# Kernel optimization log

Hardware: AMD Instinct MI355X
Metric: run time of the kernel (lower is better)

Reference implementation:

```python
import jax, jax.numpy as jnp
import numpy as np

RADIUS = 8
EPS = 0.0001


def box_filter_1d(x, axis, r):
    # cumsum summed-area trick; zero padding at edges (matches torch version)
    cs = jnp.swapaxes(jnp.cumsum(x, axis=axis), axis, 0)
    out = jnp.concatenate([
        cs[r:2 * r + 1],
        cs[2 * r + 1:] - cs[:-2 * r - 1],
        cs[-1:] - cs[-2 * r - 1:-r - 1],
    ], axis=0)
    return jnp.swapaxes(out, 0, axis)


def box_filter(x, r):
    for ax in range(2, x.ndim):
        x = box_filter_1d(x, ax, r)
    return x


def setup_inputs() -> dict:
    key = jax.random.key(0)
    k1, k2 = jax.random.split(key)
    I = jax.random.normal(k1, (8, 4, 768, 768), dtype=jnp.float32)
    p = jax.random.uniform(k2, (8, 1, 768, 768), dtype=jnp.float32)
    return {"I": I, "p": p}


def reference(I, p):
    r = RADIUS
    bs, c, h, w = I.shape
    f = lambda t: box_filter(t, r)

    N = f(jnp.ones_like(I[:, :1]))              # (b,1,h,w) window pixel counts
    I_mean = f(I) / N                            # (b,c,h,w)
    p_mean = f(p) / N                            # (b,1,h,w)
    Ip_mean = f(p * I) / N                       # (b,c,h,w)
    first_term = Ip_mean - p_mean * I_mean       # (b,c,h,w)

    # per-pixel cxc covariance of the guide
    cov = jnp.einsum('bchw,bdhw->bcdhw', I, I).reshape(bs, c * c, h, w)
    cov = (f(cov) / N).reshape(bs, c, c, h, w).transpose(0, 3, 4, 1, 2)  # (b,h,w,c,c)
    eps_mat = EPS * jnp.eye(c, dtype=I.dtype)
    second_term = jnp.linalg.inv(cov + eps_mat)  # batched small-matrix inverse

    # NOTE: einsum strings reproduce the original module exactly
    A = jnp.einsum('bchw,bhwcd->bchw', first_term, second_term)
    b = p_mean - jnp.einsum('bchw,bdhw->bhw', A, I_mean)[:, None]  # (b,1,h,w)

    A_mean = f(A) / N
    b_mean = f(b) / N
    q = jnp.einsum('bchw,bdhw->bhw', A_mean, I)[:, None] + b_mean
    return q
```

## Files before the change

### kernel.cpp

```cpp
#include <hip/hip_runtime.h>


#define HH 768
#define WW 768
#define CC 4
#define BB 8
#define RR 8
#define EPSF 1.0e-4f

#define TA 128
#define OUTA 112
#define SHA 24
#define NSTRIPE (HH / SHA)
#define NBAND 7

#define SHB 16
#define NSTRIPEB (HH / SHB)

__device__ __forceinline__ void loadpix(const float* __restrict__ Ib,
                                        const float* __restrict__ pb,
                                        int row, int gc, float pr[19]) {
  const int off = row * WW + gc;
  const int chs = HH * WW;
  float i0 = Ib[off];
  float i1 = Ib[chs + off];
  float i2 = Ib[2 * chs + off];
  float i3 = Ib[3 * chs + off];
  float pv = pb[off];
  pr[0] = i0; pr[1] = i1; pr[2] = i2; pr[3] = i3;
  pr[4] = pv;
  pr[5] = pv * i0; pr[6] = pv * i1; pr[7] = pv * i2; pr[8] = pv * i3;
  pr[9]  = i0 * i0; pr[10] = i0 * i1; pr[11] = i0 * i2; pr[12] = i0 * i3;
  pr[13] = i1 * i1; pr[14] = i1 * i2; pr[15] = i1 * i3;
  pr[16] = i2 * i2; pr[17] = i2 * i3;
  pr[18] = i3 * i3;
}

__global__ __launch_bounds__(TA) void gf_stageA(const float* __restrict__ I,
                                                const float* __restrict__ p,
                                                float2* __restrict__ AB,
                                                float* __restrict__ sumI_ws,
                                                int storeSum) {
  __shared__ float v[TA][20];
  __shared__ float s4[TA][20];
  const int tid = threadIdx.x;
  const int band0 = (int)blockIdx.x * OUTA;
  const int r0 = (int)blockIdx.y * SHA;
  const int batch = (int)blockIdx.z;
  const int gc = band0 - RR + tid;
  const bool colok = (gc >= 0 && gc < WW);

  const float* Ib = I + (size_t)batch * CC * HH * WW;
  const float* pb = p + (size_t)batch * HH * WW;
  float* sIb = sumI_ws + (size_t)batch * HH * WW;

  float s[20];
#pragma unroll
  for (int k = 0; k < 20; ++k) s[k] = 0.0f;

  if (colok) {
    int rlo = r0 - RR - 1; if (rlo < 0) rlo = 0;
    for (int row = rlo; row < r0 + RR; ++row) {
      float pr[19]; loadpix(Ib, pb, row, gc, pr);
#pragma unroll
      for (int k = 0; k < 19; ++k) s[k] += pr[k];
      if (storeSum && r0 == 0)
        sIb[row * WW + gc] = pr[0] + pr[1] + pr[2] + pr[3];
    }
  }

  const int oc = band0 + tid;
  const bool outok = (tid < OUTA) && (oc < WW);
  const int nw = min(oc + RR, WW - 1) - max(oc - RR, 0) + 1;

  for (int r = r0; r < r0 + SHA; ++r) {
    if (colok) {
      int rl = r + RR;
      if (rl < HH) {
        float pr[19]; loadpix(Ib, pb, rl, gc, pr);
#pragma unroll
        for (int k = 0; k < 19; ++k) s[k] += pr[k];
        if (storeSum)
          sIb[rl * WW + gc] = pr[0] + pr[1] + pr[2] + pr[3];
      }
      int rt = r - RR - 1;
      if (rt >= 0) {
        float pr[19]; loadpix(Ib, pb, rt, gc, pr);
#pragma unroll
        for (int k = 0; k < 19; ++k) s[k] -= pr[k];
      }
    }
    {
      float4* vp = (float4*)(&v[tid][0]);
      vp[0] = make_float4(s[0],  s[1],  s[2],  s[3]);
      vp[1] = make_float4(s[4],  s[5],  s[6],  s[7]);
      vp[2] = make_float4(s[8],  s[9],  s[10], s[11]);
      vp[3] = make_float4(s[12], s[13], s[14], s[15]);
      vp[4] = make_float4(s[16], s[17], s[18], 0.0f);
    }
    __syncthreads();
    float t4[20];
    if (tid < TA - 3) {
      const float* a1 = &v[tid + 1][0];
      const float* a2 = &v[tid + 2][0];
      const float* a3 = &v[tid + 3][0];
      float4* op = (float4*)(&s4[tid][0]);
#pragma unroll
      for (int j = 0; j < 5; ++j) {
        float4 xa = ((const float4*)a1)[j];
        float4 xb = ((const float4*)a2)[j];
        float4 xc = ((const float4*)a3)[j];
        float o0 = s[4*j + 0] + xa.x + xb.x + xc.x;
        float o1 = s[4*j + 1] + xa.y + xb.y + xc.y;
        float o2 = s[4*j + 2] + xa.z + xb.z + xc.z;
        float o3 = s[4*j + 3] + xa.w + xb.w + xc.w;
        op[j] = make_float4(o0, o1, o2, o3);
        t4[4*j + 0] = o0; t4[4*j + 1] = o1; t4[4*j + 2] = o2; t4[4*j + 3] = o3;
      }
    }
    __syncthreads();
    if (outok) {
      float h[20];
      const float* q4  = &s4[tid + 4][0];
      const float* q8  = &s4[tid + 8][0];
      const float* q12 = &s4[tid + 12][0];
      const float* q16 = &v[tid + 16][0];
#pragma unroll
      for (int j = 0; j < 5; ++j) {
        float4 a4 = ((const float4*)q4)[j];
        float4 b4 = ((const float4*)q8)[j];
        float4 c4 = ((const float4*)q12)[j];
        float4 d4 = ((const float4*)q16)[j];
        h[4*j + 0] = t4[4*j + 0] + a4.x + b4.x + c4.x + d4.x;
        h[4*j + 1] = t4[4*j + 1] + a4.y + b4.y + c4.y + d4.y;
        h[4*j + 2] = t4[4*j + 2] + a4.z + b4.z + c4.z + d4.z;
        h[4*j + 3] = t4[4*j + 3] + a4.w + b4.w + c4.w + d4.w;
      }
      const int nh = min(r + RR, HH - 1) - max(r - RR, 0) + 1;
      const float invN = 1.0f / (float)(nh * nw);
      float Im0 = h[0] * invN, Im1 = h[1] * invN, Im2 = h[2] * invN, Im3 = h[3] * invN;
      float pm = h[4] * invN;
      float ft0 = h[5] * invN - pm * Im0;
      float ft1 = h[6] * invN - pm * Im1;
      float ft2 = h[7] * invN - pm * Im2;
      float ft3 = h[8] * invN - pm * Im3;
      float m[4][4];
      m[0][0] = h[9]  * invN + EPSF;
      m[0][1] = h[10] * invN;
      m[0][2] = h[11] * invN;
      m[0][3] = h[12] * invN;
      m[1][1] = h[13] * invN + EPSF;
      m[1][2] = h[14] * invN;
      m[1][3] = h[15] * invN;
      m[2][2] = h[16] * invN + EPSF;
      m[2][3] = h[17] * invN;
      m[3][3] = h[18] * invN + EPSF;
      m[1][0] = m[0][1]; m[2][0] = m[0][2]; m[3][0] = m[0][3];
      m[2][1] = m[1][2]; m[3][1] = m[1][3]; m[3][2] = m[2][3];
      float y[4] = {1.0f, 1.0f, 1.0f, 1.0f};
#pragma unroll
      for (int k = 0; k < 4; ++k) {
        float piv = 1.0f / m[k][k];
#pragma unroll
        for (int j = 0; j < 4; ++j) m[k][j] *= piv;
        y[k] *= piv;
#pragma unroll
        for (int i = 0; i < 4; ++i) {
          if (i == k) continue;
          float f = m[i][k];
#pragma unroll
          for (int j = 0; j < 4; ++j) m[i][j] -= f * m[k][j];
          y[i] -= f * y[k];
        }
      }
      float Asum = ft0 * y[0] + ft1 * y[1] + ft2 * y[2] + ft3 * y[3];
      float bv = pm - Asum * (Im0 + Im1 + Im2 + Im3);
      AB[((size_t)batch * HH + r) * WW + oc] = make_float2(Asum, bv);
    }
    __syncthreads();
  }
}

__global__ __launch_bounds__(TA) void gf_stageB(const float* __restrict__ I,
                                                const float2* __restrict__ AB,
                                                const float* __restrict__ sumI_ws,
                                                float* __restrict__ q, int useSum) {
  __shared__ float2 v2[TA];
  __shared__ float2 s42[TA];
  const int tid = threadIdx.x;
  const int band0 = (int)blockIdx.x * OUTA;
  const int r0 = (int)blockIdx.y * SHB;
  const int batch = (int)blockIdx.z;
  const int gc = band0 - RR + tid;
  const bool colok = (gc >= 0 && gc < WW);

  const float2* ABb = AB + (size_t)batch * HH * WW;
  const float* sIb = sumI_ws + (size_t)batch * HH * WW;
  const float* Ib = I + (size_t)batch * CC * HH * WW;

  const int oc = band0 + tid;
  const bool outok = (tid < OUTA) && (oc < WW);
  const int nw = min(oc + RR, WW - 1) - max(oc - RR, 0) + 1;

  float2 w[SHB + 17];
#pragma unroll
  for (int k = 0; k < SHB + 17; ++k) {
    const int row = r0 - RR - 1 + k;
    const bool ok = colok && (row >= 0) && (row < HH);
    w[k] = ok ? ABb[row * WW + gc] : make_float2(0.0f, 0.0f);
  }
  float sm[SHB];
  if (useSum) {
#pragma unroll
    for (int j = 0; j < SHB; ++j)
      sm[j] = outok ? sIb[(r0 + j) * WW + oc] : 0.0f;
  }

  float sA = 0.0f, sB = 0.0f;
#pragma unroll
  for (int k = 0; k < 17; ++k) { sA += w[k].x; sB += w[k].y; }

#pragma unroll
  for (int j = 0; j < SHB; ++j) {
    const int r = r0 + j;
    sA += w[j + 17].x - w[j].x;
    sB += w[j + 17].y - w[j].y;
    v2[tid] = make_float2(sA, sB);
    __syncthreads();
    float tx = 0.0f, ty = 0.0f;
    if (tid < TA - 3) {
      float2 a = v2[tid + 1], b = v2[tid + 2], c = v2[tid + 3];
      tx = sA + a.x + b.x + c.x;
      ty = sB + a.y + b.y + c.y;
      s42[tid] = make_float2(tx, ty);
    }
    __syncthreads();
    if (outok) {
      float2 a = s42[tid + 4], b = s42[tid + 8], c = s42[tid + 12], d = v2[tid + 16];
      float hA = tx + a.x + b.x + c.x + d.x;
      float hB = ty + a.y + b.y + c.y + d.y;
      const int nh = min(r + RR, HH - 1) - max(r - RR, 0) + 1;
      const float invN = 1.0f / (float)(nh * nw);
      float sumI;
      if (useSum) {
        sumI = sm[j];
      } else {
        const int off = r * WW + oc;
        const int chs = HH * WW;
        sumI = Ib[off] + Ib[chs + off] + Ib[2 * chs + off] + Ib[3 * chs + off];
      }
      q[((size_t)batch * HH + r) * WW + oc] = (hA * sumI + hB) * invN;
    }
    __syncthreads();
  }
}

extern "C" void kernel_launch(void* const* d_in, const int* in_sizes, int n_in,
                              void* d_out, int out_size, void* d_ws, size_t ws_size,
                              hipStream_t stream) {
  const float* I = (const float*)d_in[0];
  const float* p = (const float*)d_in[1];
  float* q = (float*)d_out;

  const size_t npix = (size_t)BB * HH * WW;
  float2* AB = (float2*)d_ws;
  float* sumI_ws = (float*)(AB + npix);
  const size_t need = npix * sizeof(float2) + npix * sizeof(float);
  const int useSum = (ws_size >= need) ? 1 : 0;

  dim3 gridA(NBAND, NSTRIPE, BB);
  dim3 gridB(NBAND, NSTRIPEB, BB);
  dim3 block(TA);
  hipLaunchKernelGGL(gf_stageA, gridA, block, 0, stream, I, p, AB, sumI_ws, useSum);
  hipLaunchKernelGGL(gf_stageB, gridB, block, 0, stream, I, AB, sumI_ws, q, useSum);
}
```

Baseline: 224.1 us.

## Rewrite stage B as 2D shared-memory tiled box filter

```diff
diff --git a/kernel.cpp b/kernel.cpp
--- a/kernel.cpp
+++ b/kernel.cpp
@@ -14,8 +14,11 @@
 #define NSTRIPE (HH / SHA)
 #define NBAND 7
 
-#define SHB 16
-#define NSTRIPEB (HH / SHB)
+#define OTW 64
+#define OTH 16
+#define STW 80
+#define STH 32
+#define TB  256
 
 __device__ __forceinline__ void loadpix(const float* __restrict__ Ib,
                                         const float* __restrict__ pb,
@@ -181,77 +184,76 @@
   }
 }
 
-__global__ __launch_bounds__(TA) void gf_stageB(const float* __restrict__ I,
+__global__ __launch_bounds__(TB) void gf_stageB(const float* __restrict__ I,
                                                 const float2* __restrict__ AB,
                                                 const float* __restrict__ sumI_ws,
                                                 float* __restrict__ q, int useSum) {
-  __shared__ float2 v2[TA];
-  __shared__ float2 s42[TA];
-  const int tid = threadIdx.x;
-  const int band0 = (int)blockIdx.x * OUTA;
-  const int r0 = (int)blockIdx.y * SHB;
+  __shared__ float2 tile[STH][STW];
+  __shared__ float2 csum[OTH][STW];
+  const int t = threadIdx.x;
+  const int bx = (int)blockIdx.x;
+  const int by = (int)blockIdx.y;
   const int batch = (int)blockIdx.z;
-  const int gc = band0 - RR + tid;
-  const bool colok = (gc >= 0 && gc < WW);
 
   const float2* ABb = AB + (size_t)batch * HH * WW;
   const float* sIb = sumI_ws + (size_t)batch * HH * WW;
   const float* Ib = I + (size_t)batch * CC * HH * WW;
 
-  const int oc = band0 + tid;
-  const bool outok = (tid < OUTA) && (oc < WW);
+  const int gx0 = bx * OTW - RR;
+  const int gy0 = by * OTH - RR;
+
+#pragma unroll
+  for (int k = 0; k < (STW * STH) / TB; ++k) {
+    const int idx = t + k * TB;
+    const int x = idx % STW;
+    const int y = idx / STW;
+    const int gx = gx0 + x;
+    const int gy = gy0 + y;
+    const bool ok = (gx >= 0) && (gx < WW) && (gy >= 0) && (gy < HH);
+    tile[y][x] = ok ? ABb[gy * WW + gx] : make_float2(0.0f, 0.0f);
+  }
+  __syncthreads();
+
+#pragma unroll
+  for (int k = 0; k < (STW * OTH) / TB; ++k) {
+    const int idx = t + k * TB;
+    const int cx = idx % STW;
+    const int cy = idx / STW;
+    float sx = 0.0f, sy = 0.0f;
+#pragma unroll
+    for (int dy = 0; dy < 17; ++dy) {
+      float2 u = tile[cy + dy][cx];
+      sx += u.x; sy += u.y;
+    }
+    csum[cy][cx] = make_float2(sx, sy);
+  }
+  __syncthreads();
+
+  const int tx = t & 63;
+  const int tg = t >> 6;
+  const int oc = bx * OTW + tx;
   const int nw = min(oc + RR, WW - 1) - max(oc - RR, 0) + 1;
-
-  float2 w[SHB + 17];
-#pragma unroll
-  for (int k = 0; k < SHB + 17; ++k) {
-    const int row = r0 - RR - 1 + k;
-    const bool ok = colok && (row >= 0) && (row < HH);
-    w[k] = ok ? ABb[row * WW + gc] : make_float2(0.0f, 0.0f);
-  }
-  float sm[SHB];
-  if (useSum) {
-#pragma unroll
-    for (int j = 0; j < SHB; ++j)
-      sm[j] = outok ? sIb[(r0 + j) * WW + oc] : 0.0f;
-  }
-
-  float sA = 0.0f, sB = 0.0f;
-#pragma unroll
-  for (int k = 0; k < 17; ++k) { sA += w[k].x; sB += w[k].y; }
-
-#pragma unroll
-  for (int j = 0; j < SHB; ++j) {
-    const int r = r0 + j;
-    sA += w[j + 17].x - w[j].x;
-    sB += w[j + 17].y - w[j].y;
-    v2[tid] = make_float2(sA, sB);
-    __syncthreads();
-    float tx = 0.0f, ty = 0.0f;
-    if (tid < TA - 3) {
-      float2 a = v2[tid + 1], b = v2[tid + 2], c = v2[tid + 3];
-      tx = sA + a.x + b.x + c.x;
-      ty = sB + a.y + b.y + c.y;
-      s42[tid] = make_float2(tx, ty);
-    }
-    __syncthreads();
-    if (outok) {
-      float2 a = s42[tid + 4], b = s42[tid + 8], c = s42[tid + 12], d = v2[tid + 16];
-      float hA = tx + a.x + b.x + c.x + d.x;
-      float hB = ty + a.y + b.y + c.y + d.y;
-      const int nh = min(r + RR, HH - 1) - max(r - RR, 0) + 1;
-      const float invN = 1.0f / (float)(nh * nw);
-      float sumI;
-      if (useSum) {
-        sumI = sm[j];
-      } else {
-        const int off = r * WW + oc;
-        const int chs = HH * WW;
-        sumI = Ib[off] + Ib[chs + off] + Ib[2 * chs + off] + Ib[3 * chs + off];
-      }
-      q[((size_t)batch * HH + r) * WW + oc] = (hA * sumI + hB) * invN;
-    }
-    __syncthreads();
+#pragma unroll
+  for (int k = 0; k < 4; ++k) {
+    const int rl = tg * 4 + k;
+    const int ro = by * OTH + rl;
+    float hx = 0.0f, hy = 0.0f;
+#pragma unroll
+    for (int dx = 0; dx < 17; ++dx) {
+      float2 u = csum[rl][tx + dx];
+      hx += u.x; hy += u.y;
+    }
+    const int nh = min(ro + RR, HH - 1) - max(ro - RR, 0) + 1;
+    const float invN = 1.0f / (float)(nh * nw);
+    float sumI;
+    if (useSum) {
+      sumI = sIb[ro * WW + oc];
+    } else {
+      const int off = ro * WW + oc;
+      const int chs = HH * WW;
+      sumI = Ib[off] + Ib[chs + off] + Ib[2 * chs + off] + Ib[3 * chs + off];
+    }
+    q[((size_t)batch * HH + ro) * WW + oc] = (hx * sumI + hy) * invN;
   }
 }
 
@@ -269,8 +271,9 @@
   const int useSum = (ws_size >= need) ? 1 : 0;
 
   dim3 gridA(NBAND, NSTRIPE, BB);
-  dim3 gridB(NBAND, NSTRIPEB, BB);
-  dim3 block(TA);
-  hipLaunchKernelGGL(gf_stageA, gridA, block, 0, stream, I, p, AB, sumI_ws, useSum);
-  hipLaunchKernelGGL(gf_stageB, gridB, block, 0, stream, I, AB, sumI_ws, q, useSum);
-}
+  dim3 gridB(WW / OTW, HH / OTH, BB);
+  dim3 blockA(TA);
+  dim3 blockB(TB);
+  hipLaunchKernelGGL(gf_stageA, gridA, blockA, 0, stream, I, p, AB, sumI_ws, useSum);
+  hipLaunchKernelGGL(gf_stageB, gridB, blockB, 0, stream, I, AB, sumI_ws, q, useSum);
+}
```

Measured after the change: 233.3 us. 1.04x slower.
